# Kernel optimization log

Hardware: AMD Instinct MI355X
Metric: run time of the kernel (lower is better)

## Reference

```python
import jax, jax.numpy as jnp
import numpy as np

RESOLUTION = 7
RATIOS = (0.25, 0.125, 0.0625, 0.03125)  # spatial scales for P2..P5
SAMPLE_RATIO = 2
BASE_SIZE = 224.0
BASE_LEVEL = 4.0
LEVEL_MIN = 2.0  # -log2(1/4)
LEVEL_MAX = 5.0  # -log2(1/32)
EPS = 1e-6
IMG = 800.0


def _make_boxes(key, n):
    k1, k2, k3, k4 = jax.random.split(key, 4)
    # log-uniform box sizes in [16, 512] px so rois hit all FPN levels
    w = jnp.exp2(jax.random.uniform(k1, (n,), minval=4.0, maxval=9.0))
    h = jnp.exp2(jax.random.uniform(k2, (n,), minval=4.0, maxval=9.0))
    cx = jax.random.uniform(k3, (n,), minval=0.0, maxval=IMG)
    cy = jax.random.uniform(k4, (n,), minval=0.0, maxval=IMG)
    x1 = jnp.clip(cx - w / 2, 0.0, IMG - 1)
    y1 = jnp.clip(cy - h / 2, 0.0, IMG - 1)
    x2 = jnp.clip(cx + w / 2, 0.0, IMG - 1)
    y2 = jnp.clip(cy + h / 2, 0.0, IMG - 1)
    return jnp.stack([x1, y1, jnp.maximum(x2, x1), jnp.maximum(y2, y1)], axis=1)


def setup_inputs() -> dict:
    key = jax.random.key(0)
    ks = jax.random.split(key, 8)
    N, C = 2, 256
    sizes = [(200, 200), (100, 100), (50, 50), (25, 25), (13, 13)]
    feats = {f"feat{i}": jax.random.normal(ks[i], (N, C, h, w), dtype=jnp.float32)
             for i, (h, w) in enumerate(sizes)}
    feats["props0"] = _make_boxes(ks[5], 512)
    feats["props1"] = _make_boxes(ks[6], 512)
    return feats


def _axis_interp(v, size):
    """Per-axis bilinear setup, matching torchvision RoIAlign (aligned=False)."""
    valid = (v >= -1.0) & (v <= size)
    v0 = jnp.maximum(v, 0.0)
    lo = jnp.floor(v0).astype(jnp.int32)
    at_edge = lo >= size - 1
    lo = jnp.where(at_edge, size - 1, lo)
    hi = jnp.where(at_edge, size - 1, lo + 1)
    frac = jnp.where(at_edge, 0.0, v0 - lo.astype(v.dtype))
    return lo, hi, frac, valid


def _roi_align(feat, rois, scale, res=RESOLUTION, sr=SAMPLE_RATIO):
    """feat: [N,C,H,W], rois: [R,5] (batch_idx,x1,y1,x2,y2) -> [R,C,res,res]."""
    N, C, H, W = feat.shape
    b = rois[:, 0].astype(jnp.int32)
    x1, y1, x2, y2 = (rois[:, 1] * scale, rois[:, 2] * scale,
                      rois[:, 3] * scale, rois[:, 4] * scale)
    roi_w = jnp.maximum(x2 - x1, 1.0)
    roi_h = jnp.maximum(y2 - y1, 1.0)
    bin_w = roi_w / res
    bin_h = roi_h / res
    P = res * sr
    offs = (jnp.arange(P, dtype=jnp.float32) + 0.5) / sr  # sample offsets in bin units
    ys = y1[:, None] + offs[None, :] * bin_h[:, None]  # [R,P]
    xs = x1[:, None] + offs[None, :] * bin_w[:, None]  # [R,P]
    yl, yh, fy, vy = _axis_interp(ys, H)
    xl, xh, fx, vx = _axis_interp(xs, W)
    bi = b[:, None, None]

    def g(yi, xi):  # gather corner values -> [R,P,P,C]
        return feat[bi, :, yi[:, :, None], xi[:, None, :]]

    hy, hx = 1.0 - fy, 1.0 - fx
    val = (g(yl, xl) * (hy[:, :, None] * hx[:, None, :])[..., None]
           + g(yl, xh) * (hy[:, :, None] * fx[:, None, :])[..., None]
           + g(yh, xl) * (fy[:, :, None] * hx[:, None, :])[..., None]
           + g(yh, xh) * (fy[:, :, None] * fx[:, None, :])[..., None])
    val = jnp.where((vy[:, :, None] & vx[:, None, :])[..., None], val, 0.0)
    R = rois.shape[0]
    pooled = val.reshape(R, res, sr, res, sr, C).mean(axis=(2, 4))  # [R,res,res,C]
    return pooled.transpose(0, 3, 1, 2)


def _pool(features, proposals):
    # convert: concat proposals with batch indices -> rois [R,5]
    inds = jnp.concatenate([jnp.full((p.shape[0], 1), i, dtype=p.dtype)
                            for i, p in enumerate(proposals)], axis=0)
    boxes = jnp.concatenate(proposals, axis=0)
    rois = jnp.concatenate([inds, boxes], axis=1)
    rois = jax.lax.stop_gradient(rois)  # torchvision RoIAlign has no roi grad
    # set_level: FPN level assignment (eq.1 of FPN paper)
    areas = (rois[:, 3] - rois[:, 1] + 1) * (rois[:, 4] - rois[:, 2] + 1)
    sizes = jnp.sqrt(areas)
    levels = jnp.floor(BASE_LEVEL + jnp.log2(sizes / BASE_SIZE + EPS))
    levels = (jnp.clip(levels, LEVEL_MIN, LEVEL_MAX) - LEVEL_MIN).astype(jnp.int32)
    R, C = rois.shape[0], features[0].shape[1]
    results = jnp.zeros((R, C, RESOLUTION, RESOLUTION), dtype=boxes.dtype)
    for lvl in range(len(RATIOS)):  # forward uses features[:-1]
        pooled = _roi_align(features[lvl], rois, RATIOS[lvl])
        results = results + jnp.where((levels == lvl)[:, None, None, None], pooled, 0.0)
    return results


def reference(feat0, feat1, feat2, feat3, feat4, props0, props1):
    return _pool([feat0, feat1, feat2, feat3, feat4], [props0, props1])
```

## Files before the change

kernel.cpp:

```cpp
#include <hip/hip_runtime.h>
#include <math.h>

#define C_CH 256
#define RESO 7
#define NBIN 49
#define CHALF 128

typedef float fx4 __attribute__((ext_vector_type(4)));
typedef unsigned int ux2 __attribute__((ext_vector_type(2)));

__device__ __forceinline__ unsigned short f2bf(float f) {
  unsigned int u = __float_as_uint(f);
  u = (u + 0x7fffu + ((u >> 16) & 1u)) >> 16;
  return (unsigned short)u;
}
__device__ __forceinline__ float bf_lo(unsigned int u) { return __uint_as_float(u << 16); }
__device__ __forceinline__ float bf_hi(unsigned int u) { return __uint_as_float(u & 0xffff0000u); }

struct TArgs {
  const float* src[4];
  unsigned short* dst[4];
  int hw[4];
  int tilesx[4];
  int tbase[5];
  int total;
};

__device__ __forceinline__ void decode_tile(const TArgs& a, int T, int& l, int& hw0,
                                            int& c0, int& n, int& HW) {
  int ll = 0;
  if (T >= a.tbase[1]) ll = 1;
  if (T >= a.tbase[2]) ll = 2;
  if (T >= a.tbase[3]) ll = 3;
  const int idx = T - a.tbase[ll];
  const int txs = a.tilesx[ll];
  const int tx = idx % txs;
  const int rem = idx / txs;
  l = ll;
  hw0 = tx * 64;
  c0 = (rem & 3) * 64;
  n = rem >> 2;
  HW = a.hw[ll];
}

__device__ __forceinline__ void load_tile(const TArgs& a, int l, int hw0, int c0, int n,
                                          int HW, int lane16, int row16, fx4 v[4]) {
  const float* s = a.src[l] + (size_t)n * C_CH * HW;
  if (((HW & 3) == 0) && (hw0 + 64 <= HW)) {
#pragma unroll
    for (int i = 0; i < 4; ++i) {
      const int c_l = row16 + 16 * i;
      v[i] = __builtin_nontemporal_load(
          (const fx4*)(s + (size_t)(c0 + c_l) * HW + hw0 + lane16 * 4));
    }
  } else {
#pragma unroll
    for (int i = 0; i < 4; ++i) {
      const int c_l = row16 + 16 * i;
      const float* row = s + (size_t)(c0 + c_l) * HW;
#pragma unroll
      for (int k = 0; k < 4; ++k) {
        const int hw = hw0 + lane16 * 4 + k;
        v[i][k] = (hw < HW) ? row[hw] : 0.0f;
      }
    }
  }
}

__global__ __launch_bounds__(256) void conv_nhwc_bf16(TArgs a) {
  __shared__ float tile[64][65];
  const int t = threadIdx.x;
  const int lane16 = t & 15;
  const int row16 = t >> 4;
  const int stride = gridDim.x;

  int T = blockIdx.x;
  int l0, hw00, c00, n0, HW0;
  decode_tile(a, T, l0, hw00, c00, n0, HW0);
  fx4 v[4];
  load_tile(a, l0, hw00, c00, n0, HW0, lane16, row16, v);

  while (true) {
    __syncthreads();
#pragma unroll
    for (int i = 0; i < 4; ++i) {
      const int c_l = row16 + 16 * i;
      tile[c_l][lane16 * 4 + 0] = v[i][0];
      tile[c_l][lane16 * 4 + 1] = v[i][1];
      tile[c_l][lane16 * 4 + 2] = v[i][2];
      tile[c_l][lane16 * 4 + 3] = v[i][3];
    }

    const int Tn = T + stride;
    const bool more = Tn < a.total;
    int l1, hw01, c01, n1, HW1;
    fx4 w[4];
    if (more) {
      decode_tile(a, Tn, l1, hw01, c01, n1, HW1);
      load_tile(a, l1, hw01, c01, n1, HW1, lane16, row16, w);
    }
    __syncthreads();

    unsigned short* d = a.dst[l0] + (size_t)n0 * HW0 * C_CH;
#pragma unroll
    for (int i = 0; i < 4; ++i) {
      const int hw_l = row16 + 16 * i;
      const int hww = hw00 + hw_l;
      if (hww < HW0) {
        const int c4 = lane16 * 4;
        ux2 p;
        p.x = (unsigned int)f2bf(tile[c4 + 0][hw_l]) |
              ((unsigned int)f2bf(tile[c4 + 1][hw_l]) << 16);
        p.y = (unsigned int)f2bf(tile[c4 + 2][hw_l]) |
              ((unsigned int)f2bf(tile[c4 + 3][hw_l]) << 16);
        *(ux2*)(d + (size_t)hww * C_CH + c00 + c4) = p;
      }
    }

    if (!more) break;
    T = Tn;
    l0 = l1; hw00 = hw01; c00 = c01; n0 = n1; HW0 = HW1;
#pragma unroll
    for (int i = 0; i < 4; ++i) v[i] = w[i];
  }
}

__global__ __launch_bounds__(512, 8) void roi_gather_bf16(
    const unsigned short* __restrict__ f0, const unsigned short* __restrict__ f1,
    const unsigned short* __restrict__ f2, const unsigned short* __restrict__ f3,
    const float* __restrict__ props0, const float* __restrict__ props1,
    float* __restrict__ out) {
  __shared__ float obuf[CHALF * NBIN];
  __shared__ int s_o0[2][14], s_o1[2][14];
  __shared__ float s_w0[2][14], s_w1[2][14];

  const int bid = blockIdx.x;
  const int r = bid >> 1;
  const int p = bid & 1;
  const int t = threadIdx.x;
  const int b = (r >= 512) ? 1 : 0;
  const float* pr = (b ? props1 : props0) + (r & 511) * 4;
  const float x1 = pr[0], y1 = pr[1], x2 = pr[2], y2 = pr[3];

  const float size = sqrtf((x2 - x1 + 1.0f) * (y2 - y1 + 1.0f));
  float lv = floorf(4.0f + log2f(size / 224.0f + 1e-6f));
  lv = fminf(fmaxf(lv, 2.0f), 5.0f) - 2.0f;
  const int lvl = (int)lv;

  const int Htab[4] = {200, 100, 50, 25};
  const float stab[4] = {0.25f, 0.125f, 0.0625f, 0.03125f};
  const int H = Htab[lvl];
  const int W = H;
  const float sc = stab[lvl];
  const unsigned short* fl = (lvl == 0) ? f0 : (lvl == 1) ? f1 : (lvl == 2) ? f2 : f3;

  const float rx1 = x1 * sc, ry1 = y1 * sc;
  const float roi_w = fmaxf(x2 * sc - rx1, 1.0f);
  const float roi_h = fmaxf(y2 * sc - ry1, 1.0f);
  const float bw = roi_w / 7.0f, bh = roi_h / 7.0f;

  if (t < 28) {
    const int axis = t / 14;
    const int k = t % 14;
    const float off = ((float)k + 0.5f) * 0.5f;
    const float v = axis ? (rx1 + off * bw) : (ry1 + off * bh);
    const int isz = H;
    const bool valid = (v >= -1.0f) && (v <= (float)isz);
    const float v0 = fmaxf(v, 0.0f);
    int lo = (int)floorf(v0);
    const bool edge = (lo >= isz - 1);
    lo = edge ? isz - 1 : lo;
    const int hi = edge ? isz - 1 : lo + 1;
    const float fr = edge ? 0.0f : (v0 - (float)lo);
    const int mul = axis ? C_CH : W * C_CH;
    const float wsc = axis ? 1.0f : 0.25f;
    s_o0[axis][k] = lo * mul;
    s_o1[axis][k] = hi * mul;
    s_w1[axis][k] = valid ? fr * wsc : 0.0f;
    s_w0[axis][k] = valid ? (1.0f - fr) * wsc : 0.0f;
  }
  __syncthreads();

  const int wv = t >> 6;
  const int ln = t & 63;
  const int cg = ln & 15;
  const int sub = ln >> 4;
  const int xt = sub & 1;
  const int yt = sub >> 1;
  const size_t HWp = (size_t)H * W;
  const unsigned short* base = fl + (size_t)b * HWp * C_CH + p * CHALF + cg * 8;

  for (int bb = wv; bb < NBIN; bb += 8) {
    const int ph = bb / 7, pw = bb - ph * 7;
    float acc[8] = {0.f, 0.f, 0.f, 0.f, 0.f, 0.f, 0.f, 0.f};
#pragma unroll
    for (int s1 = 0; s1 < 2; ++s1) {
      const int sy = 2 * ph + s1;
      const int yo = yt ? s_o1[0][sy] : s_o0[0][sy];
      const float wy = yt ? s_w1[0][sy] : s_w0[0][sy];
#pragma unroll
      for (int s2 = 0; s2 < 2; ++s2) {
        const int sx = 2 * pw + s2;
        const int xo = xt ? s_o1[1][sx] : s_o0[1][sx];
        const float wx = xt ? s_w1[1][sx] : s_w0[1][sx];
        const uint4 q = *(const uint4*)(base + yo + xo);
        const float w = wy * wx;
        acc[0] = fmaf(bf_lo(q.x), w, acc[0]);
        acc[1] = fmaf(bf_hi(q.x), w, acc[1]);
        acc[2] = fmaf(bf_lo(q.y), w, acc[2]);
        acc[3] = fmaf(bf_hi(q.y), w, acc[3]);
        acc[4] = fmaf(bf_lo(q.z), w, acc[4]);
        acc[5] = fmaf(bf_hi(q.z), w, acc[5]);
        acc[6] = fmaf(bf_lo(q.w), w, acc[6]);
        acc[7] = fmaf(bf_hi(q.w), w, acc[7]);
      }
    }
#pragma unroll
    for (int k = 0; k < 8; ++k) {
      acc[k] += __shfl_xor(acc[k], 16);
      acc[k] += __shfl_xor(acc[k], 32);
    }
    const int c0 = cg * 8 + sub * 2;
    obuf[(c0 + 0) * NBIN + bb] = acc[sub * 2 + 0];
    obuf[(c0 + 1) * NBIN + bb] = acc[sub * 2 + 1];
  }
  __syncthreads();

  fx4* o4 = (fx4*)(out + (size_t)r * (NBIN * C_CH) + (size_t)p * (CHALF * NBIN));
  const fx4* ob4 = (const fx4*)obuf;
  for (int i = t; i < CHALF * NBIN / 4; i += 512)
    __builtin_nontemporal_store(ob4[i], o4 + i);
}

__global__ __launch_bounds__(256) void roi_gather_nchw(
    const float* __restrict__ f0, const float* __restrict__ f1,
    const float* __restrict__ f2, const float* __restrict__ f3,
    const float* __restrict__ props0, const float* __restrict__ props1,
    float* __restrict__ out) {
  __shared__ float obuf[NBIN * C_CH];
  __shared__ int s_o0[2][14], s_o1[2][14];
  __shared__ float s_w0[2][14], s_w1[2][14];

  const int r = blockIdx.x;
  const int t = threadIdx.x;
  const int b = (r >= 512) ? 1 : 0;
  const float* pr = (b ? props1 : props0) + (r & 511) * 4;
  const float x1 = pr[0], y1 = pr[1], x2 = pr[2], y2 = pr[3];
  const float size = sqrtf((x2 - x1 + 1.0f) * (y2 - y1 + 1.0f));
  float lv = floorf(4.0f + log2f(size / 224.0f + 1e-6f));
  lv = fminf(fmaxf(lv, 2.0f), 5.0f) - 2.0f;
  const int lvl = (int)lv;
  const int Htab[4] = {200, 100, 50, 25};
  const float stab[4] = {0.25f, 0.125f, 0.0625f, 0.03125f};
  const int H = Htab[lvl];
  const int W = H;
  const float sc = stab[lvl];
  const float* fl = (lvl == 0) ? f0 : (lvl == 1) ? f1 : (lvl == 2) ? f2 : f3;
  const float rx1 = x1 * sc, ry1 = y1 * sc;
  const float roi_w = fmaxf(x2 * sc - rx1, 1.0f);
  const float roi_h = fmaxf(y2 * sc - ry1, 1.0f);
  const float bw = roi_w / 7.0f, bh = roi_h / 7.0f;
  if (t < 28) {
    const int axis = t / 14;
    const int k = t % 14;
    const float off = ((float)k + 0.5f) * 0.5f;
    const float v = axis ? (rx1 + off * bw) : (ry1 + off * bh);
    const int isz = H;
    const bool valid = (v >= -1.0f) && (v <= (float)isz);
    const float v0 = fmaxf(v, 0.0f);
    int lo = (int)floorf(v0);
    const bool edge = (lo >= isz - 1);
    lo = edge ? isz - 1 : lo;
    const int hi = edge ? isz - 1 : lo + 1;
    const float fr = edge ? 0.0f : (v0 - (float)lo);
    const int mul = axis ? 1 : W;
    s_o0[axis][k] = lo * mul;
    s_o1[axis][k] = hi * mul;
    s_w1[axis][k] = valid ? fr : 0.0f;
    s_w0[axis][k] = valid ? (1.0f - fr) : 0.0f;
  }
  __syncthreads();
  const int wv = t >> 6;
  const int ln = t & 63;
  const size_t HWp = (size_t)H * W;
  const float* base = fl + ((size_t)b * C_CH + ln * 4) * HWp;
  for (int bb = wv; bb < NBIN; bb += 4) {
    const int ph = bb / 7, pw = bb - ph * 7;
    float4 acc = make_float4(0.f, 0.f, 0.f, 0.f);
    for (int s1 = 0; s1 < 2; ++s1) {
      const int sy = 2 * ph + s1;
      const int yo0 = s_o0[0][sy], yo1 = s_o1[0][sy];
      const float wy0 = s_w0[0][sy], wy1 = s_w1[0][sy];
      for (int s2 = 0; s2 < 2; ++s2) {
        const int sx = 2 * pw + s2;
        const int xo0 = s_o0[1][sx], xo1 = s_o1[1][sx];
        const float w00 = wy0 * s_w0[1][sx], w01 = wy0 * s_w1[1][sx];
        const float w10 = wy1 * s_w0[1][sx], w11 = wy1 * s_w1[1][sx];
        float e[4];
        for (int j = 0; j < 4; ++j) {
          e[j] = w00 * base[j * HWp + yo0 + xo0] + w01 * base[j * HWp + yo0 + xo1] +
                 w10 * base[j * HWp + yo1 + xo0] + w11 * base[j * HWp + yo1 + xo1];
        }
        acc.x += e[0]; acc.y += e[1]; acc.z += e[2]; acc.w += e[3];
      }
    }
    const int c4 = ln * 4;
    obuf[(c4 + 0) * NBIN + bb] = acc.x * 0.25f;
    obuf[(c4 + 1) * NBIN + bb] = acc.y * 0.25f;
    obuf[(c4 + 2) * NBIN + bb] = acc.z * 0.25f;
    obuf[(c4 + 3) * NBIN + bb] = acc.w * 0.25f;
  }
  __syncthreads();
  float4* o4 = (float4*)(out + (size_t)r * (NBIN * C_CH));
  const float4* ob4 = (const float4*)obuf;
  for (int i = t; i < NBIN * C_CH / 4; i += 256) o4[i] = ob4[i];
}

extern "C" void kernel_launch(void* const* d_in, const int* in_sizes, int n_in,
                              void* d_out, int out_size, void* d_ws, size_t ws_size,
                              hipStream_t stream) {
  const float* f0 = (const float*)d_in[0];
  const float* f1 = (const float*)d_in[1];
  const float* f2 = (const float*)d_in[2];
  const float* f3 = (const float*)d_in[3];
  const float* p0 = (const float*)d_in[5];
  const float* p1 = (const float*)d_in[6];
  float* out = (float*)d_out;
  unsigned short* ws = (unsigned short*)d_ws;

  const int HWs[4] = {200 * 200, 100 * 100, 50 * 50, 25 * 25};
  size_t off[4];
  size_t acc = 0;
  for (int l = 0; l < 4; ++l) {
    off[l] = acc;
    acc += (size_t)2 * C_CH * HWs[l];
  }
  const size_t need_bytes = acc * sizeof(unsigned short);

  if (ws_size >= need_bytes) {
    TArgs a;
    a.src[0] = f0; a.src[1] = f1; a.src[2] = f2; a.src[3] = f3;
    int cum = 0;
    for (int l = 0; l < 4; ++l) {
      a.dst[l] = ws + off[l];
      a.hw[l] = HWs[l];
      a.tilesx[l] = (HWs[l] + 63) / 64;
      a.tbase[l] = cum;
      cum += a.tilesx[l] * 4 * 2;
    }
    a.tbase[4] = cum;
    a.total = cum;
    const int nblocks = (cum < 2048) ? cum : 2048;
    conv_nhwc_bf16<<<nblocks, 256, 0, stream>>>(a);
    roi_gather_bf16<<<2048, 512, 0, stream>>>(a.dst[0], a.dst[1], a.dst[2], a.dst[3],
                                              p0, p1, out);
  } else {
    roi_gather_nchw<<<1024, 256, 0, stream>>>(f0, f1, f2, f3, p0, p1, out);
  }
}
```

Before: 189.2 us.

## Assign all four bilinear corners per thread in ROI gather, drop shuffles

The bf16 ROI gather kernel now gives each thread one (bin, 8-channel group) work item and has it load and accumulate all four bilinear corners itself. Before, four lanes each took one corner and were combined with cross-lane shuffles. Block size drops from 512 to 256 threads. This removes the shuffle reductions and gives more independent loads per thread for memory-level parallelism. The cost is more registers per thread, and the obuf stores now write 8 channels per thread at stride NBIN, which may cause LDS bank conflicts.

```diff
diff --git a/kernel.cpp b/kernel.cpp
--- a/kernel.cpp
+++ b/kernel.cpp
@@ -125,7 +125,7 @@
   }
 }
 
-__global__ __launch_bounds__(512, 8) void roi_gather_bf16(
+__global__ __launch_bounds__(256) void roi_gather_bf16(
     const unsigned short* __restrict__ f0, const unsigned short* __restrict__ f1,
     const unsigned short* __restrict__ f2, const unsigned short* __restrict__ f3,
     const float* __restrict__ props0, const float* __restrict__ props1,
@@ -181,54 +181,75 @@
   }
   __syncthreads();
 
-  const int wv = t >> 6;
-  const int ln = t & 63;
-  const int cg = ln & 15;
-  const int sub = ln >> 4;
-  const int xt = sub & 1;
-  const int yt = sub >> 1;
   const size_t HWp = (size_t)H * W;
-  const unsigned short* base = fl + (size_t)b * HWp * C_CH + p * CHALF + cg * 8;
-
-  for (int bb = wv; bb < NBIN; bb += 8) {
+  const unsigned short* baseR = fl + (size_t)b * HWp * C_CH + p * CHALF;
+
+  for (int ti = t; ti < NBIN * 16; ti += 256) {
+    const int bb = ti >> 4;
+    const int cg = ti & 15;
     const int ph = bb / 7, pw = bb - ph * 7;
+    const unsigned short* bp = baseR + cg * 8;
     float acc[8] = {0.f, 0.f, 0.f, 0.f, 0.f, 0.f, 0.f, 0.f};
 #pragma unroll
     for (int s1 = 0; s1 < 2; ++s1) {
       const int sy = 2 * ph + s1;
-      const int yo = yt ? s_o1[0][sy] : s_o0[0][sy];
-      const float wy = yt ? s_w1[0][sy] : s_w0[0][sy];
+      const int yo0 = s_o0[0][sy], yo1 = s_o1[0][sy];
+      const float wy0 = s_w0[0][sy], wy1 = s_w1[0][sy];
 #pragma unroll
       for (int s2 = 0; s2 < 2; ++s2) {
         const int sx = 2 * pw + s2;
-        const int xo = xt ? s_o1[1][sx] : s_o0[1][sx];
-        const float wx = xt ? s_w1[1][sx] : s_w0[1][sx];
-        const uint4 q = *(const uint4*)(base + yo + xo);
-        const float w = wy * wx;
-        acc[0] = fmaf(bf_lo(q.x), w, acc[0]);
-        acc[1] = fmaf(bf_hi(q.x), w, acc[1]);
-        acc[2] = fmaf(bf_lo(q.y), w, acc[2]);
-        acc[3] = fmaf(bf_hi(q.y), w, acc[3]);
-        acc[4] = fmaf(bf_lo(q.z), w, acc[4]);
-        acc[5] = fmaf(bf_hi(q.z), w, acc[5]);
-        acc[6] = fmaf(bf_lo(q.w), w, acc[6]);
-        acc[7] = fmaf(bf_hi(q.w), w, acc[7]);
+        const int xo0 = s_o0[1][sx], xo1 = s_o1[1][sx];
+        const float wx0 = s_w0[1][sx], wx1 = s_w1[1][sx];
+        const uint4 q00 = *(const uint4*)(bp + yo0 + xo0);
+        const uint4 q01 = *(const uint4*)(bp + yo0 + xo1);
+        const uint4 q10 = *(const uint4*)(bp + yo1 + xo0);
+        const uint4 q11 = *(const uint4*)(bp + yo1 + xo1);
+        const float w00 = wy0 * wx0, w01 = wy0 * wx1;
+        const float w10 = wy1 * wx0, w11 = wy1 * wx1;
+        acc[0] = fmaf(bf_lo(q00.x), w00, acc[0]);
+        acc[1] = fmaf(bf_hi(q00.x), w00, acc[1]);
+        acc[2] = fmaf(bf_lo(q00.y), w00, acc[2]);
+        acc[3] = fmaf(bf_hi(q00.y), w00, acc[3]);
+        acc[4] = fmaf(bf_lo(q00.z), w00, acc[4]);
+        acc[5] = fmaf(bf_hi(q00.z), w00, acc[5]);
+        acc[6] = fmaf(bf_lo(q00.w), w00, acc[6]);
+        acc[7] = fmaf(bf_hi(q00.w), w00, acc[7]);
+        acc[0] = fmaf(bf_lo(q01.x), w01, acc[0]);
+        acc[1] = fmaf(bf_hi(q01.x), w01, acc[1]);
+        acc[2] = fmaf(bf_lo(q01.y), w01, acc[2]);
+        acc[3] = fmaf(bf_hi(q01.y), w01, acc[3]);
+        acc[4] = fmaf(bf_lo(q01.z), w01, acc[4]);
+        acc[5] = fmaf(bf_hi(q01.z), w01, acc[5]);
+        acc[6] = fmaf(bf_lo(q01.w), w01, acc[6]);
+        acc[7] = fmaf(bf_hi(q01.w), w01, acc[7]);
+        acc[0] = fmaf(bf_lo(q10.x), w10, acc[0]);
+        acc[1] = fmaf(bf_hi(q10.x), w10, acc[1]);
+        acc[2] = fmaf(bf_lo(q10.y), w10, acc[2]);
+        acc[3] = fmaf(bf_hi(q10.y), w10, acc[3]);
+        acc[4] = fmaf(bf_lo(q10.z), w10, acc[4]);
+        acc[5] = fmaf(bf_hi(q10.z), w10, acc[5]);
+        acc[6] = fmaf(bf_lo(q10.w), w10, acc[6]);
+        acc[7] = fmaf(bf_hi(q10.w), w10, acc[7]);
+        acc[0] = fmaf(bf_lo(q11.x), w11, acc[0]);
+        acc[1] = fmaf(bf_hi(q11.x), w11, acc[1]);
+        acc[2] = fmaf(bf_lo(q11.y), w11, acc[2]);
+        acc[3] = fmaf(bf_hi(q11.y), w11, acc[3]);
+        acc[4] = fmaf(bf_lo(q11.z), w11, acc[4]);
+        acc[5] = fmaf(bf_hi(q11.z), w11, acc[5]);
+        acc[6] = fmaf(bf_lo(q11.w), w11, acc[6]);
+        acc[7] = fmaf(bf_hi(q11.w), w11, acc[7]);
       }
     }
-#pragma unroll
-    for (int k = 0; k < 8; ++k) {
-      acc[k] += __shfl_xor(acc[k], 16);
-      acc[k] += __shfl_xor(acc[k], 32);
-    }
-    const int c0 = cg * 8 + sub * 2;
-    obuf[(c0 + 0) * NBIN + bb] = acc[sub * 2 + 0];
-    obuf[(c0 + 1) * NBIN + bb] = acc[sub * 2 + 1];
+    const int c0 = cg * 8;
+#pragma unroll
+    for (int k = 0; k < 8; ++k)
+      obuf[(c0 + k) * NBIN + bb] = acc[k];
   }
   __syncthreads();
 
   fx4* o4 = (fx4*)(out + (size_t)r * (NBIN * C_CH) + (size_t)p * (CHALF * NBIN));
   const fx4* ob4 = (const fx4*)obuf;
-  for (int i = t; i < CHALF * NBIN / 4; i += 512)
+  for (int i = t; i < CHALF * NBIN / 4; i += 256)
     __builtin_nontemporal_store(ob4[i], o4 + i);
 }
 
@@ -352,7 +373,7 @@
     a.total = cum;
     const int nblocks = (cum < 2048) ? cum : 2048;
     conv_nhwc_bf16<<<nblocks, 256, 0, stream>>>(a);
-    roi_gather_bf16<<<2048, 512, 0, stream>>>(a.dst[0], a.dst[1], a.dst[2], a.dst[3],
+    roi_gather_bf16<<<2048, 256, 0, stream>>>(a.dst[0], a.dst[1], a.dst[2], a.dst[3],
                                               p0, p1, out);
   } else {
     roi_gather_nchw<<<1024, 256, 0, stream>>>(f0, f1, f2, f3, p0, p1, out);
```

New measurement: 187.7 us. No clear change (-0.8%).
